# Performance work log

Hardware: AMD Instinct MI355X
Metric: run time of the kernel (lower is better)

The kernel has to match this reference:

```python
import jax, jax.numpy as jnp
import numpy as np

D_INP=36; D_MODEL=144; NHEAD=4; NHID=128; NLAYERS=2
MAX_LEN=215; D_STATIC=9; D_PE=16; N_CLASSES=2; B=128
D_OB=D_MODEL//D_INP; GCH=MAX_LEN*D_OB; D_TR=D_MODEL+D_PE; D_FINAL=D_TR+D_INP
_EI=np.stack(np.nonzero(np.ones((D_INP,D_INP),dtype=np.int64)))  # torch.nonzero(ones).T -> all pairs
SRC_N=jnp.asarray(_EI[0]); TGT_N=jnp.asarray(_EI[1]); N_EDGE=_EI.shape[1]


def setup_inputs():
    ks=jax.random.split(jax.random.key(0),40)
    def w(i,shape,s=0.05): return jax.random.normal(ks[i],shape,jnp.float32)*s
    return {
      'src': jax.random.normal(ks[0],(MAX_LEN,B,2*D_INP),jnp.float32),
      'static': jax.random.normal(ks[1],(B,D_STATIC),jnp.float32),
      'times': jax.random.uniform(ks[2],(MAX_LEN,B),jnp.float32)*MAX_LEN,
      'lengths': jax.random.randint(ks[3],(B,),32,MAX_LEN+1),
      'R_u': w(4,(1,D_INP*D_OB)),
      'emb_w': w(5,(D_INP,D_STATIC)), 'emb_b': jnp.zeros(D_INP,jnp.float32),
      'Wv1': w(6,(GCH,GCH),1.0/np.sqrt(GCH)), 'bv1': jnp.zeros(GCH,jnp.float32),
      'Wv2': w(7,(GCH,GCH),1.0/np.sqrt(GCH)), 'bv2': jnp.zeros(GCH,jnp.float32),
      'in_proj_w': w(8,(NLAYERS,3*D_TR,D_TR)), 'in_proj_b': jnp.zeros((NLAYERS,3*D_TR),jnp.float32),
      'out_w': w(9,(NLAYERS,D_TR,D_TR)), 'out_b': jnp.zeros((NLAYERS,D_TR),jnp.float32),
      'lin1_w': w(10,(NLAYERS,NHID,D_TR)), 'lin1_b': jnp.zeros((NLAYERS,NHID),jnp.float32),
      'lin2_w': w(11,(NLAYERS,D_TR,NHID)), 'lin2_b': jnp.zeros((NLAYERS,D_TR),jnp.float32),
      'ln1_s': jnp.ones((NLAYERS,D_TR),jnp.float32), 'ln1_b': jnp.zeros((NLAYERS,D_TR),jnp.float32),
      'ln2_s': jnp.ones((NLAYERS,D_TR),jnp.float32), 'ln2_b': jnp.zeros((NLAYERS,D_TR),jnp.float32),
      'mlp1_w': w(12,(D_FINAL,D_FINAL)), 'mlp1_b': jnp.zeros(D_FINAL,jnp.float32),
      'mlp2_w': w(13,(N_CLASSES,D_FINAL)), 'mlp2_b': jnp.zeros(N_CLASSES,jnp.float32),
    }


def _seg_softmax(wgt, seg, n):
    m=jnp.full((n,),-jnp.inf,wgt.dtype).at[seg].max(wgt)
    e=jnp.exp(wgt-m[seg])
    s=jnp.zeros((n,),wgt.dtype).at[seg].add(e)
    return e/s[seg]


def _ln(x,s,b):
    mu=jnp.mean(x,-1,keepdims=True); v=jnp.var(x,-1,keepdims=True)
    return (x-mu)/jnp.sqrt(v+1e-5)*s+b


def _forward(src, static, times, R_u, emb_w, emb_b, Wv1, bv1, Wv2, bv2, in_proj_w, in_proj_b, out_w, out_b, lin1_w, lin1_b, lin2_w, lin2_b, ln1_s, ln1_b, ln2_s, ln2_b, mlp1_w, mlp1_b, mlp2_w, mlp2_b, lengths):
    T,Bb=src.shape[0],src.shape[1]
    obs=src[:,:,:D_INP]                                  # drop mask half
    h=jax.nn.relu(jnp.repeat(obs,D_OB,axis=-1)*R_u)      # h_u = relu(x_u*R_u), [T,B,144]
    ts=jnp.asarray(MAX_LEN**np.linspace(0,1,D_PE//2),jnp.float32)
    scaled=times[:,:,None]/ts
    pe=jnp.concatenate([jnp.sin(scaled),jnp.cos(scaled)],-1)  # [T,B,16]
    emb=static@emb_w.T+emb_b                             # [B,36]
    # --- Observation_progation x2 (use_beta=False): gather-softmax-scatter per sensor graph ---
    xb=h.transpose(1,0,2).reshape(Bb,T,D_INP,D_OB).transpose(0,2,1,3).reshape(Bb,D_INP,GCH)
    ew=jnp.ones((N_EDGE,),jnp.float32)                   # adj=ones -> edge_weights=1
    gamma=_seg_softmax(ew,TGT_N,D_INP)                   # softmax over edges per target node
    def prop(x_,Wv,bv):
        V=jax.nn.relu(x_@Wv.T+bv)                        # relu(lin_value(x_j))
        msgs=V[:,SRC_N,:]*gamma[None,:,None]             # gather source features per edge
        return jnp.zeros_like(x_).at[:,TGT_N,:].add(msgs)  # scatter-add to targets
    x1=prop(xb,Wv1,bv1)
    x2=prop(x1,Wv2,bv2)                                  # layer2 uses alpha1 = raw edge_weights
    alpha=jnp.broadcast_to(ew[None,:],(Bb,N_EDGE))       # alpha_all.T
    sq=jnp.sum(alpha*alpha,1)
    d2=jnp.maximum(sq[:,None]+sq[None,:]-2.0*(alpha@alpha.T),0.0)
    distance=jnp.mean(jnp.sqrt(d2))
    out=x2.reshape(Bb,D_INP,T,D_OB).transpose(2,0,1,3).reshape(T,Bb,D_INP*D_OB)
    x=jnp.concatenate([out,pe],-1)                       # [T,B,160]
    mask=jnp.arange(T)[None,:]>=lengths[:,None]          # [B,T] True = padded
    hd=D_TR//NHEAD
    for l in range(NLAYERS):                             # torch post-norm TransformerEncoderLayer
        qkv=x@in_proj_w[l].T+in_proj_b[l]
        q,k,v=jnp.split(qkv,3,-1)
        def heads(t): return t.reshape(T,Bb,NHEAD,hd).transpose(1,2,0,3)  # [B,H,T,hd]
        sc=jnp.einsum('bhqd,bhkd->bhqk',heads(q),heads(k))/np.sqrt(hd)
        sc=jnp.where(mask[:,None,None,:],jnp.float32(-1e30),sc)
        o=jnp.einsum('bhqk,bhkd->bhqd',jax.nn.softmax(sc,-1),heads(v))
        o=o.transpose(2,0,1,3).reshape(T,Bb,D_TR)@out_w[l].T+out_b[l]
        x=_ln(x+o,ln1_s[l],ln1_b[l])
        ff=jax.nn.relu(x@lin1_w[l].T+lin1_b[l])@lin2_w[l].T+lin2_b[l]
        x=_ln(x+ff,ln2_s[l],ln2_b[l])
    valid=1.0-mask.T[:,:,None].astype(x.dtype)           # [T,B,1]
    agg=jnp.sum(x*valid,0)/(lengths[:,None].astype(x.dtype)+1.0)
    feat=jnp.concatenate([agg,emb],1)                    # [B,196]
    logits=jax.nn.relu(feat@mlp1_w.T+mlp1_b)@mlp2_w.T+mlp2_b
    return logits,distance


def reference(src, static, times, lengths, R_u, emb_w, emb_b, Wv1, bv1, Wv2, bv2, in_proj_w, in_proj_b, out_w, out_b, lin1_w, lin1_b, lin2_w, lin2_b, ln1_s, ln1_b, ln2_s, ln2_b, mlp1_w, mlp1_b, mlp2_w, mlp2_b):
    return _forward(src, static, times, R_u, emb_w, emb_b, Wv1, bv1, Wv2, bv2, in_proj_w, in_proj_b, out_w, out_b, lin1_w, lin1_b, lin2_w, lin2_b, ln1_s, ln1_b, ln2_s, ln2_b, mlp1_w, mlp1_b, mlp2_w, mlp2_b, lengths)
```

## Files before the change

### kernel.cpp

```cpp
#include <hip/hip_runtime.h>
#include <math.h>

#define T_LEN 215
#define TP    224
#define B_N   128
#define DINP  36
#define D_TR  160
#define HD    40
#define D_FIN 196
#define KPG   864

typedef __attribute__((ext_vector_type(8))) short short8v;
typedef __attribute__((ext_vector_type(4))) float f32x4;

__device__ __forceinline__ ushort f2bf(float x) {
  union { float f; unsigned u; } c; c.f = x;
  unsigned r = c.u + 0x7fffu + ((c.u >> 16) & 1u);
  return (ushort)(r >> 16);
}
__device__ __forceinline__ float bf2f(ushort h) {
  union { unsigned u; float f; } c; c.u = ((unsigned)h) << 16;
  return c.f;
}

__global__ __launch_bounds__(256) void k_prep(const float* __restrict__ Wv1,
    const float* __restrict__ Wv2, const float* __restrict__ ipw, const float* __restrict__ ow,
    const float* __restrict__ l1w, const float* __restrict__ l2w,
    const float* __restrict__ src, const float* __restrict__ R_u,
    const float* __restrict__ stat, const float* __restrict__ emb_w, const float* __restrict__ emb_b,
    ushort* __restrict__ wv1b, ushort* __restrict__ wv2b, ushort* __restrict__ ipwb,
    ushort* __restrict__ owb, ushort* __restrict__ l1wb, ushort* __restrict__ l2wb,
    float* __restrict__ v2acc, float* __restrict__ featacc, ushort* __restrict__ obuf16,
    ushort* __restrict__ xb16) {
  __shared__ float Ss[T_LEN * DINP];
  if (blockIdx.x >= 8202) {
    const int b = blockIdx.x - 8202, tid = threadIdx.x;
    for (int i = tid; i < T_LEN * DINP; i += 256) {
      int t = i / DINP, j = i - t * DINP;
      Ss[i] = src[((size_t)t * B_N + b) * 72 + j];
    }
    __syncthreads();
    for (int i = tid; i < DINP * T_LEN; i += 256) {
      int ii = i / T_LEN, t = i - ii * T_LEN;
      float v = Ss[t * DINP + ii];
      float4 r = ((const float4*)R_u)[ii];
      ushort4 o;
      o.x = f2bf(fmaxf(v * r.x, 0.f)); o.y = f2bf(fmaxf(v * r.y, 0.f));
      o.z = f2bf(fmaxf(v * r.z, 0.f)); o.w = f2bf(fmaxf(v * r.w, 0.f));
      ushort* row = xb16 + (size_t)(b * DINP + ii) * KPG;
      *(ushort4*)(row + 4 * t) = o;
      if (t == 0) { ushort4 z = {0, 0, 0, 0}; *(ushort4*)(row + 860) = z; }
    }
    return;
  }
  int i = blockIdx.x * 256 + threadIdx.x;
  if (i < 746496) { int n = i / KPG, k = i % KPG;
    wv1b[i] = (n < 860 && k < 860) ? f2bf(Wv1[n * 860 + k]) : (ushort)0; return; }
  i -= 746496;
  if (i < 746496) { int n = i / KPG, k = i % KPG;
    wv2b[i] = (n < 860 && k < 860) ? f2bf(Wv2[n * 860 + k]) : (ushort)0; return; }
  i -= 746496;
  if (i < 153600) { ipwb[i] = f2bf(ipw[i]); return; }
  i -= 153600;
  if (i < 51200)  { owb[i] = f2bf(ow[i]); return; }
  i -= 51200;
  if (i < 40960)  { l1wb[i] = f2bf(l1w[i]); return; }
  i -= 40960;
  if (i < 40960)  { l2wb[i] = f2bf(l2w[i]); return; }
  i -= 40960;
  if (i < 110592) { v2acc[i] = 0.f; return; }
  i -= 110592;
  if (i < 20480)  { int b = i / D_TR, d = i - b * D_TR;
    featacc[b * D_FIN + d] = 0.f; return; }
  i -= 20480;
  if (i < 4608)   { int b = i / DINP, ii = i - b * DINP;
    float s = emb_b[ii];
    #pragma unroll
    for (int k = 0; k < 9; k++) s = fmaf(stat[b * 9 + k], emb_w[ii * 9 + k], s);
    featacc[b * D_FIN + D_TR + ii] = s; return; }
  i -= 4608;
  if (i < 184320) {
    int b = i / 1440, rem = i % 1440;
    int t = 215 + rem / 160, cc = rem % 160;
    obuf16[((size_t)b * TP + t) * D_TR + cc] = 0; return;
  }
}

__global__ __launch_bounds__(256) void k_red_s1(const ushort* __restrict__ V1b, ushort* __restrict__ s1) {
  int idx = blockIdx.x * 256 + threadIdx.x;
  if (idx >= B_N * KPG) return;
  int b = idx / KPG, n = idx % KPG;
  float s = 0.f;
  if (n < 860) {
    #pragma unroll 4
    for (int i = 0; i < DINP; i++) s += bf2f(V1b[((size_t)b * DINP + i) * 860 + n]);
    s *= (1.0f / 36.0f);
  }
  s1[idx] = (n < 860) ? f2bf(s) : (ushort)0;
}

__global__ __launch_bounds__(256) void k_buildx(const float* __restrict__ v2acc,
    const float* __restrict__ bv2, const float* __restrict__ times,
    ushort* __restrict__ x16) {
  int idx = blockIdx.x * 256 + threadIdx.x;
  if (idx >= B_N * TP * 40) return;
  int c = idx % 40;
  int r = idx / 40;
  int t = r % TP, b = r / TP;
  float4 f = {0.f, 0.f, 0.f, 0.f};
  if (t < T_LEN) {
    if (c < 36) {
      float4 a = *(const float4*)&v2acc[(size_t)b * KPG + 4 * t];
      float4 bb = *(const float4*)&bv2[4 * t];
      f.x = fmaxf(a.x + bb.x, 0.f); f.y = fmaxf(a.y + bb.y, 0.f);
      f.z = fmaxf(a.z + bb.z, 0.f); f.w = fmaxf(a.w + bb.w, 0.f);
    } else {
      float tm = times[t * B_N + b];
      int j0 = (c - 36) * 4;
      bool is_sin = j0 < 8;
      int kb = j0 & 7;
      float o[4];
      #pragma unroll
      for (int qq = 0; qq < 4; qq++) {
        float ts = expf((float)(kb + qq) * 0.76723400f);
        float sc = tm / ts;
        o[qq] = is_sin ? sinf(sc) : cosf(sc);
      }
      f.x = o[0]; f.y = o[1]; f.z = o[2]; f.w = o[3];
    }
  }
  ushort4 h = {f2bf(f.x), f2bf(f.y), f2bf(f.z), f2bf(f.w)};
  *(ushort4*)(x16 + (size_t)r * D_TR + 4 * c) = h;
}

template <int RELU, int SPLIT, int WMODE, int BNT>
__global__ __launch_bounds__(256) void gemm_bf16(const ushort* __restrict__ A,
    const ushort* __restrict__ W, const float* __restrict__ bias, void* __restrict__ Cv,
    int KP, int ldc, int ncols, int kts) {
  __shared__ ushort As[128 * 32];
  __shared__ ushort Ws[BNT * 32];
  constexpr int NJ = BNT / 16;
  const int tid = threadIdx.x;
  const int wave = tid >> 6, lane = tid & 63;
  const int lr = lane & 15, hi = lane >> 4;
  const int m0 = blockIdx.y * 128, n0 = blockIdx.x * BNT;
  const int kt0 = blockIdx.z * kts;

  f32x4 acc[2][NJ];
  #pragma unroll
  for (int i = 0; i < 2; i++)
    #pragma unroll
    for (int j = 0; j < NJ; j++) acc[i][j] = (f32x4){0.f, 0.f, 0.f, 0.f};

  const int ar = tid >> 2, g = tid & 3;
  const size_t abase0 = (size_t)(m0 + ar) * KP;
  const size_t abase1 = (size_t)(m0 + ar + 64) * KP;
  const size_t bbase0 = (size_t)(n0 + ar) * KP;
  const size_t bbase1 = (size_t)(n0 + ar + 64) * KP;
  const int awb0 = ar * 64 + ((g * 16) ^ ((ar & 3) << 4));
  const int awb1 = awb0 + 64 * 64;

  const int arow0 = wave * 32 + lr;
  const int arb0 = arow0 * 64 + ((hi * 16) ^ ((arow0 & 3) << 4));
  const int arb1 = (arow0 + 16) * 64 + ((hi * 16) ^ (((arow0 + 16) & 3) << 4));
  int brb[NJ];
  #pragma unroll
  for (int j = 0; j < NJ; j++)
    brb[j] = (j * 16 + lr) * 64 + ((hi * 16) ^ ((lr & 3) << 4));

  for (int kt = 0; kt < kts; ++kt) {
    const int k0 = (kt0 + kt) * 32;
    uint4 va0 = *(const uint4*)(A + abase0 + k0 + g * 8);
    uint4 va1 = *(const uint4*)(A + abase1 + k0 + g * 8);
    uint4 vb0 = *(const uint4*)(W + bbase0 + k0 + g * 8);
    uint4 vb1;
    if constexpr (BNT == 128) vb1 = *(const uint4*)(W + bbase1 + k0 + g * 8);
    if (kt) __syncthreads();
    *(uint4*)((char*)As + awb0) = va0;
    *(uint4*)((char*)As + awb1) = va1;
    *(uint4*)((char*)Ws + awb0) = vb0;
    if constexpr (BNT == 128) *(uint4*)((char*)Ws + awb1) = vb1;
    __syncthreads();
    short8v a0 = *(const short8v*)((const char*)As + arb0);
    short8v a1 = *(const short8v*)((const char*)As + arb1);
    #pragma unroll
    for (int j = 0; j < NJ; j++) {
      short8v bf = *(const short8v*)((const char*)Ws + brb[j]);
      acc[0][j] = __builtin_amdgcn_mfma_f32_16x16x32_bf16(a0, bf, acc[0][j], 0, 0, 0);
      acc[1][j] = __builtin_amdgcn_mfma_f32_16x16x32_bf16(a1, bf, acc[1][j], 0, 0, 0);
    }
  }

  #pragma unroll
  for (int i = 0; i < 2; i++) {
    #pragma unroll
    for (int j = 0; j < NJ; j++) {
      int col = n0 + j * 16 + lr;
      int row = m0 + wave * 32 + i * 16 + hi * 4;
      if (col < ncols) {
        if (SPLIT) {
          #pragma unroll
          for (int r = 0; r < 4; r++)
            atomicAdd((float*)Cv + (size_t)(row + r) * ldc + col, acc[i][j][r]);
        } else {
          float bb = bias ? bias[col] : 0.f;
          #pragma unroll
          for (int r = 0; r < 4; r++) {
            float xv = acc[i][j][r] + bb;
            if (RELU) xv = fmaxf(xv, 0.f);
            if (WMODE == 0) ((float*)Cv)[(size_t)(row + r) * ldc + col] = xv;
            else            ((ushort*)Cv)[(size_t)(row + r) * ldc + col] = f2bf(xv);
          }
        }
      }
    }
  }
}

__global__ __launch_bounds__(256) void gemm_qkv(const ushort* __restrict__ A,
    const ushort* __restrict__ W, const float* __restrict__ bias,
    ushort* __restrict__ qkvB, ushort* __restrict__ Vt, int kts) {
  __shared__ ushort As[128 * 32];
  __shared__ ushort Ws[128 * 32];
  const int KP = 160;
  const int tid = threadIdx.x;
  const int wave = tid >> 6, lane = tid & 63;
  const int lr = lane & 15, hi = lane >> 4;
  const int m0 = blockIdx.y * 128, n0 = blockIdx.x * 128;

  f32x4 acc[2][8];
  #pragma unroll
  for (int i = 0; i < 2; i++)
    #pragma unroll
    for (int j = 0; j < 8; j++) acc[i][j] = (f32x4){0.f, 0.f, 0.f, 0.f};

  const int ar = tid >> 2, g = tid & 3;
  const size_t abase0 = (size_t)(m0 + ar) * KP;
  const size_t abase1 = (size_t)(m0 + ar + 64) * KP;
  const size_t bbase0 = (size_t)(n0 + ar) * KP;
  const size_t bbase1 = (size_t)(n0 + ar + 64) * KP;
  const int awb0 = ar * 64 + ((g * 16) ^ ((ar & 3) << 4));
  const int awb1 = awb0 + 64 * 64;

  const int arow0 = wave * 32 + lr;
  const int arb0 = arow0 * 64 + ((hi * 16) ^ ((arow0 & 3) << 4));
  const int arb1 = (arow0 + 16) * 64 + ((hi * 16) ^ (((arow0 + 16) & 3) << 4));
  int brb[8];
  #pragma unroll
  for (int j = 0; j < 8; j++)
    brb[j] = (j * 16 + lr) * 64 + ((hi * 16) ^ ((lr & 3) << 4));

  for (int kt = 0; kt < kts; ++kt) {
    const int k0 = kt * 32;
    uint4 va0 = *(const uint4*)(A + abase0 + k0 + g * 8);
    uint4 va1 = *(const uint4*)(A + abase1 + k0 + g * 8);
    uint4 vb0 = *(const uint4*)(W + bbase0 + k0 + g * 8);
    uint4 vb1 = *(const uint4*)(W + bbase1 + k0 + g * 8);
    if (kt) __syncthreads();
    *(uint4*)((char*)As + awb0) = va0;
    *(uint4*)((char*)As + awb1) = va1;
    *(uint4*)((char*)Ws + awb0) = vb0;
    *(uint4*)((char*)Ws + awb1) = vb1;
    __syncthreads();
    short8v a0 = *(const short8v*)((const char*)As + arb0);
    short8v a1 = *(const short8v*)((const char*)As + arb1);
    #pragma unroll
    for (int j = 0; j < 8; j++) {
      short8v bf = *(const short8v*)((const char*)Ws + brb[j]);
      acc[0][j] = __builtin_amdgcn_mfma_f32_16x16x32_bf16(a0, bf, acc[0][j], 0, 0, 0);
      acc[1][j] = __builtin_amdgcn_mfma_f32_16x16x32_bf16(a1, bf, acc[1][j], 0, 0, 0);
    }
  }

  #pragma unroll
  for (int i = 0; i < 2; i++) {
    const int row = m0 + wave * 32 + i * 16 + hi * 4;
    const int b = row / TP, t0 = row - b * TP;
    #pragma unroll
    for (int j = 0; j < 8; j++) {
      int col = n0 + j * 16 + lr;
      if (col < 320) {
        float bb = bias[col];
        #pragma unroll
        for (int r = 0; r < 4; r++)
          qkvB[(size_t)(row + r) * 480 + col] = f2bf(acc[i][j][r] + bb);
      } else if (col < 480) {
        float bb = bias[col];
        int dg = col - 320;
        int hh = dg / 40, dd = dg - hh * 40;
        ushort4 pv;
        pv.x = f2bf(acc[i][j][0] + bb); pv.y = f2bf(acc[i][j][1] + bb);
        pv.z = f2bf(acc[i][j][2] + bb); pv.w = f2bf(acc[i][j][3] + bb);
        *(ushort4*)(Vt + (((size_t)(b * 4 + hh) * 48 + dd) * TP + t0)) = pv;
      }
    }
  }
}

__global__ __launch_bounds__(256) void gemm_ln(const ushort* __restrict__ A,
    const ushort* __restrict__ W, const float* __restrict__ bias,
    const float* __restrict__ gam, const float* __restrict__ bet,
    ushort* __restrict__ x16, int KP, int kts,
    const int* __restrict__ lengths, float* __restrict__ featacc) {
  __shared__ ushort As[64 * 32];
  __shared__ ushort Ws[160 * 32];
  const int tid = threadIdx.x;
  const int wave = tid >> 6, lane = tid & 63;
  const int lr = lane & 15, hi = lane >> 4;
  const int m0 = blockIdx.x * 64;

  f32x4 acc[10];
  #pragma unroll
  for (int j = 0; j < 10; j++) acc[j] = (f32x4){0.f, 0.f, 0.f, 0.f};

  const int ar = tid >> 2, g = tid & 3;
  const size_t abase = (size_t)(m0 + ar) * KP;
  const int awb = ar * 64 + ((g * 16) ^ ((ar & 3) << 4));
  const int wr0 = tid >> 2,         ws0 = tid & 3;
  const int wr1 = (tid + 256) >> 2, ws1 = (tid + 256) & 3;
  const int wr2 = (tid + 512) >> 2, ws2 = (tid + 512) & 3;
  const int wwb0 = wr0 * 64 + ((ws0 * 16) ^ ((wr0 & 3) << 4));
  const int wwb1 = wr1 * 64 + ((ws1 * 16) ^ ((wr1 & 3) << 4));
  const int wwb2 = wr2 * 64 + ((ws2 * 16) ^ ((wr2 & 3) << 4));

  const int arow = wave * 16 + lr;
  const int arb = arow * 64 + ((hi * 16) ^ ((arow & 3) << 4));
  int brb[10];
  #pragma unroll
  for (int j = 0; j < 10; j++)
    brb[j] = (j * 16 + lr) * 64 + ((hi * 16) ^ ((lr & 3) << 4));

  for (int kt = 0; kt < kts; ++kt) {
    const int k0 = kt * 32;
    uint4 va = *(const uint4*)(A + abase + k0 + g * 8);
    uint4 w0 = *(const uint4*)(W + (size_t)wr0 * KP + k0 + ws0 * 8);
    uint4 w1 = *(const uint4*)(W + (size_t)wr1 * KP + k0 + ws1 * 8);
    uint4 w2;
    if (tid < 128) w2 = *(const uint4*)(W + (size_t)wr2 * KP + k0 + ws2 * 8);
    if (kt) __syncthreads();
    *(uint4*)((char*)As + awb) = va;
    *(uint4*)((char*)Ws + wwb0) = w0;
    *(uint4*)((char*)Ws + wwb1) = w1;
    if (tid < 128) *(uint4*)((char*)Ws + wwb2) = w2;
    __syncthreads();
    short8v a0 = *(const short8v*)((const char*)As + arb);
    #pragma unroll
    for (int j = 0; j < 10; j++) {
      short8v bf = *(const short8v*)((const char*)Ws + brb[j]);
      acc[j] = __builtin_amdgcn_mfma_f32_16x16x32_bf16(a0, bf, acc[j], 0, 0, 0);
    }
  }

  const int rb = m0 + wave * 16 + hi * 4;
  float s[4] = {0.f, 0.f, 0.f, 0.f};
  #pragma unroll
  for (int j = 0; j < 10; j++) {
    const int col = j * 16 + lr;
    const float bb = bias[col];
    #pragma unroll
    for (int r = 0; r < 4; r++) {
      float v = acc[j][r] + bb + bf2f(x16[(size_t)(rb + r) * D_TR + col]);
      acc[j][r] = v;
      s[r] += v;
    }
  }
  #pragma unroll
  for (int r = 0; r < 4; r++) {
    s[r] += __shfl_xor(s[r], 1, 64);
    s[r] += __shfl_xor(s[r], 2, 64);
    s[r] += __shfl_xor(s[r], 4, 64);
    s[r] += __shfl_xor(s[r], 8, 64);
  }
  float mu[4], q2[4] = {0.f, 0.f, 0.f, 0.f};
  #pragma unroll
  for (int r = 0; r < 4; r++) mu[r] = s[r] * (1.0f / 160.0f);
  #pragma unroll
  for (int j = 0; j < 10; j++)
    #pragma unroll
    for (int r = 0; r < 4; r++) {
      float d = acc[j][r] - mu[r];
      q2[r] += d * d;
    }
  #pragma unroll
  for (int r = 0; r < 4; r++) {
    q2[r] += __shfl_xor(q2[r], 1, 64);
    q2[r] += __shfl_xor(q2[r], 2, 64);
    q2[r] += __shfl_xor(q2[r], 4, 64);
    q2[r] += __shfl_xor(q2[r], 8, 64);
  }
  float rstd[4];
  #pragma unroll
  for (int r = 0; r < 4; r++) rstd[r] = rsqrtf(q2[r] * (1.0f / 160.0f) + 1e-5f);

  if (featacc == nullptr) {
    #pragma unroll
    for (int j = 0; j < 10; j++) {
      const int col = j * 16 + lr;
      const float gc = gam[col], bc = bet[col];
      #pragma unroll
      for (int r = 0; r < 4; r++) {
        float o = (acc[j][r] - mu[r]) * rstd[r] * gc + bc;
        x16[(size_t)(rb + r) * D_TR + col] = f2bf(o);
      }
    }
  } else {
    const int b = rb / TP, t0 = rb - b * TP;
    int L = lengths[b]; if (L > T_LEN) L = T_LEN;
    #pragma unroll
    for (int j = 0; j < 10; j++) {
      const int col = j * 16 + lr;
      const float gc = gam[col], bc = bet[col];
      float sacc = 0.f;
      #pragma unroll
      for (int r = 0; r < 4; r++) {
        float o = (acc[j][r] - mu[r]) * rstd[r] * gc + bc;
        if (t0 + r < L) sacc += o;
      }
      if (t0 < L) atomicAdd(&featacc[b * D_FIN + col], sacc);
    }
  }
}

__global__ __launch_bounds__(64) void k_attn4(const ushort* __restrict__ qkvB,
    const ushort* __restrict__ Vt, const int* __restrict__ lengths,
    ushort* __restrict__ o16) {
  __shared__ ushort SP[16 * 232];
  const int bh = blockIdx.x;
  const int b = bh >> 2, h = bh & 3;
  int L = lengths[b]; if (L > T_LEN) L = T_LEN;
  const int q0 = blockIdx.y << 4;
  if (q0 >= L) return;
  const int lane = threadIdx.x;
  const int lr = lane & 15, hi = lane >> 4;
  const int nk16 = (L + 15) >> 4;
  const int nkt  = (L + 31) >> 5;
  const float SC = 0.15811388300841898f;

  const ushort* qrow = qkvB + ((size_t)b * TP + q0) * 480 + h * 40;
  uint4 qa0u = *(const uint4*)(qrow + lr * 480 + hi * 8);
  uint4 qa1u = {0, 0, 0, 0};
  if (hi == 0) qa1u = *(const uint4*)(qrow + lr * 480 + 32);
  short8v qa0 = *(short8v*)&qa0u;
  short8v qa1 = *(short8v*)&qa1u;

  f32x4 c[14];
  #pragma unroll
  for (int kt = 0; kt < 14; ++kt) {
    c[kt] = (f32x4){0.f, 0.f, 0.f, 0.f};
    if (kt < nk16) {
      const ushort* krow = qkvB + ((size_t)b * TP + kt * 16) * 480 + 160 + h * 40;
      uint4 kb0u = *(const uint4*)(krow + lr * 480 + hi * 8);
      uint4 kb1u = {0, 0, 0, 0};
      if (hi == 0) kb1u = *(const uint4*)(krow + lr * 480 + 32);
      c[kt] = __builtin_amdgcn_mfma_f32_16x16x32_bf16(qa0, *(short8v*)&kb0u, c[kt], 0, 0, 0);
      c[kt] = __builtin_amdgcn_mfma_f32_16x16x32_bf16(qa1, *(short8v*)&kb1u, c[kt], 0, 0, 0);
    }
  }

  float mx[4] = {-1e30f, -1e30f, -1e30f, -1e30f};
  #pragma unroll
  for (int kt = 0; kt < 14; ++kt) {
    if (kt < nk16) {
      bool valid = (kt * 16 + lr) < L;
      #pragma unroll
      for (int r = 0; r < 4; r++) {
        float v = valid ? c[kt][r] : -1e30f;
        mx[r] = fmaxf(mx[r], v);
      }
    }
  }
  #pragma unroll
  for (int r = 0; r < 4; r++) {
    mx[r] = fmaxf(mx[r], __shfl_xor(mx[r], 1, 64));
    mx[r] = fmaxf(mx[r], __shfl_xor(mx[r], 2, 64));
    mx[r] = fmaxf(mx[r], __shfl_xor(mx[r], 4, 64));
    mx[r] = fmaxf(mx[r], __shfl_xor(mx[r], 8, 64));
  }
  float sum[4] = {0.f, 0.f, 0.f, 0.f};
  #pragma unroll
  for (int kt = 0; kt < 14; ++kt) {
    if (kt < nk16) {
      bool valid = (kt * 16 + lr) < L;
      #pragma unroll
      for (int r = 0; r < 4; r++) {
        float p = valid ? __expf(SC * (c[kt][r] - mx[r])) : 0.f;
        sum[r] += p;
        c[kt][r] = p;
      }
    }
  }
  #pragma unroll
  for (int r = 0; r < 4; r++) {
    sum[r] += __shfl_xor(sum[r], 1, 64);
    sum[r] += __shfl_xor(sum[r], 2, 64);
    sum[r] += __shfl_xor(sum[r], 4, 64);
    sum[r] += __shfl_xor(sum[r], 8, 64);
  }

  const int nk16w = nkt * 2;
  #pragma unroll
  for (int kt = 0; kt < 14; ++kt) {
    if (kt < nk16w) {
      #pragma unroll
      for (int r = 0; r < 4; r++)
        SP[(hi * 4 + r) * 232 + kt * 16 + lr] = f2bf(c[kt][r]);
    }
  }
  __syncthreads();

  f32x4 o0 = {0.f, 0.f, 0.f, 0.f}, o1 = o0, o2 = o0;
  const ushort* vbase = Vt + (size_t)bh * 48 * TP;
  #pragma unroll
  for (int kt = 0; kt < 7; ++kt) {
    if (kt < nkt) {
      short8v pa = *(const short8v*)((const char*)SP + lr * 464 + kt * 64 + hi * 16);
      const ushort* vb = vbase + kt * 32 + hi * 8;
      short8v v0 = *(const short8v*)(vb + (size_t)lr * TP);
      short8v v1 = *(const short8v*)(vb + (size_t)(16 + lr) * TP);
      short8v v2 = *(const short8v*)(vb + (size_t)(32 + lr) * TP);
      o0 = __builtin_amdgcn_mfma_f32_16x16x32_bf16(pa, v0, o0, 0, 0, 0);
      o1 = __builtin_amdgcn_mfma_f32_16x16x32_bf16(pa, v1, o1, 0, 0, 0);
      o2 = __builtin_amdgcn_mfma_f32_16x16x32_bf16(pa, v2, o2, 0, 0, 0);
    }
  }

  #pragma unroll
  for (int r = 0; r < 4; r++) {
    int t = q0 + hi * 4 + r;
    if (t < T_LEN) {
      float inv = 1.0f / sum[r];
      ushort* op = o16 + ((size_t)b * TP + t) * D_TR + h * 40;
      op[lr]      = f2bf(o0[r] * inv);
      op[16 + lr] = f2bf(o1[r] * inv);
      if (lr < 8) op[32 + lr] = f2bf(o2[r] * inv);
    }
  }
}

__global__ __launch_bounds__(256) void k_head2(const float* __restrict__ featacc,
    const int* __restrict__ lengths, const float* __restrict__ m1w,
    const float* __restrict__ m1b, const float* __restrict__ m2w,
    const float* __restrict__ m2b, float* __restrict__ out) {
  __shared__ float feat[196];
  __shared__ float m1o_s[196];
  __shared__ float r0[4], r1[4];
  const int b = blockIdx.x, tid = threadIdx.x;
  int L = lengths[b]; if (L > T_LEN) L = T_LEN;
  const float inv = 1.0f / (float)(L + 1);
  if (tid < D_FIN)
    feat[tid] = featacc[(size_t)b * D_FIN + tid] * (tid < D_TR ? inv : 1.f);
  __syncthreads();
  if (tid < D_FIN) {
    float s = m1b[tid];
    const float* wr = m1w + (size_t)tid * D_FIN;
    #pragma unroll 4
    for (int k = 0; k < D_FIN; k++) s = fmaf(feat[k], wr[k], s);
    m1o_s[tid] = fmaxf(s, 0.f);
  }
  __syncthreads();
  float p0 = 0.f, p1 = 0.f;
  if (tid < D_FIN) {
    p0 = m1o_s[tid] * m2w[tid];
    p1 = m1o_s[tid] * m2w[D_FIN + tid];
  }
  #pragma unroll
  for (int off = 32; off; off >>= 1) {
    p0 += __shfl_xor(p0, off, 64);
    p1 += __shfl_xor(p1, off, 64);
  }
  int w = tid >> 6;
  if ((tid & 63) == 0) { r0[w] = p0; r1[w] = p1; }
  __syncthreads();
  if (tid == 0) out[2 * b]     = r0[0] + r0[1] + r0[2] + r0[3] + m2b[0];
  if (tid == 1) out[2 * b + 1] = r1[0] + r1[1] + r1[2] + r1[3] + m2b[1];
  if (b == 0 && tid == 2) out[256] = 0.f;
}

extern "C" void kernel_launch(void* const* d_in, const int* in_sizes, int n_in,
                              void* d_out, int out_size, void* d_ws, size_t ws_size,
                              hipStream_t stream) {
  const float* src   = (const float*)d_in[0];
  const float* stat  = (const float*)d_in[1];
  const float* times = (const float*)d_in[2];
  const int*   lens  = (const int*)d_in[3];
  const float* R_u   = (const float*)d_in[4];
  const float* emb_w = (const float*)d_in[5];
  const float* emb_b = (const float*)d_in[6];
  const float* Wv1   = (const float*)d_in[7];
  const float* bv1   = (const float*)d_in[8];
  const float* Wv2   = (const float*)d_in[9];
  const float* bv2   = (const float*)d_in[10];
  const float* ipw   = (const float*)d_in[11];
  const float* ipb   = (const float*)d_in[12];
  const float* ow    = (const float*)d_in[13];
  const float* ob    = (const float*)d_in[14];
  const float* l1w   = (const float*)d_in[15];
  const float* l1b   = (const float*)d_in[16];
  const float* l2w   = (const float*)d_in[17];
  const float* l2b   = (const float*)d_in[18];
  const float* ln1s  = (const float*)d_in[19];
  const float* ln1bb = (const float*)d_in[20];
  const float* ln2s  = (const float*)d_in[21];
  const float* ln2bb = (const float*)d_in[22];
  const float* m1w   = (const float*)d_in[23];
  const float* m1b   = (const float*)d_in[24];
  const float* m2w   = (const float*)d_in[25];
  const float* m2b   = (const float*)d_in[26];
  float* out = (float*)d_out;

  char* p = (char*)d_ws;
  ushort* x16    = (ushort*)p;  p += 9175040;
  float*  v2acc  = (float*)p;   p += 442368;
  ushort* s1b    = (ushort*)p;  p += 221184;
  ushort* obuf16 = (ushort*)p;  p += 9175040;
  ushort* wv1b   = (ushort*)p;  p += 1492992;
  ushort* wv2b   = (ushort*)p;  p += 1492992;
  ushort* ipwb   = (ushort*)p;  p += 307200;
  ushort* owb    = (ushort*)p;  p += 102400;
  ushort* l1wb   = (ushort*)p;  p += 81920;
  ushort* l2wb   = (ushort*)p;  p += 81920;
  float*  featacc= (float*)p;   p += 100352;
  char*   R2     = p;
  ushort* xb16   = (ushort*)R2;
  ushort* V1b    = (ushort*)(R2 + 7962624);
  ushort* qkvB   = (ushort*)R2;
  ushort* ffb16  = (ushort*)R2;
  ushort* Vt     = (ushort*)(R2 + 27525120);

  k_prep<<<8330, 256, 0, stream>>>(Wv1, Wv2, ipw, ow, l1w, l2w, src, R_u,
                                   stat, emb_w, emb_b,
                                   wv1b, wv2b, ipwb, owb, l1wb, l2wb,
                                   v2acc, featacc, obuf16, xb16);

  gemm_bf16<1, 0, 1, 128><<<dim3(7, 36, 1), 256, 0, stream>>>(
      xb16, wv1b, bv1, V1b, KPG, 860, 860, 27);
  k_red_s1<<<432, 256, 0, stream>>>(V1b, s1b);
  gemm_bf16<0, 1, 0, 64><<<dim3(14, 1, 9), 256, 0, stream>>>(
      s1b, wv2b, nullptr, v2acc, KPG, KPG, KPG, 3);
  k_buildx<<<4480, 256, 0, stream>>>(v2acc, bv2, times, x16);

  for (int l = 0; l < 2; l++) {
    gemm_qkv<<<dim3(4, 224, 1), 256, 0, stream>>>(
        x16, ipwb + (size_t)l * 76800, ipb + l * 480, qkvB, Vt, 5);
    k_attn4<<<dim3(512, 14), 64, 0, stream>>>(qkvB, Vt, lens, obuf16);
    gemm_ln<<<448, 256, 0, stream>>>(obuf16, owb + (size_t)l * 25600, ob + l * 160,
                                     ln1s + l * 160, ln1bb + l * 160, x16, 160, 5,
                                     lens, nullptr);
    gemm_bf16<1, 0, 1, 64><<<dim3(2, 224, 1), 256, 0, stream>>>(
        x16, l1wb + (size_t)l * 20480, l1b + l * 128, ffb16, 160, 128, 128, 5);
    gemm_ln<<<448, 256, 0, stream>>>(ffb16, l2wb + (size_t)l * 20480, l2b + l * 160,
                                     ln2s + l * 160, ln2bb + l * 160, x16, 128, 4,
                                     lens, (l == 1) ? featacc : nullptr);
  }

  k_head2<<<128, 256, 0, stream>>>(featacc, lens, m1w, m1b, m2w, m2b, out);
}
```

Before: 248.1 us.

## Fuse node-mean reduction into GEMM epilogue and fuse FFN two-GEMM block

The first GEMM now applies bias and ReLU and atomically accumulates the mean over the 36 nodes into a float buffer, so the V1 intermediate and the separate reduction kernel are no longer needed. The second GEMM reads that float buffer directly, converting to bf16 with the 1/36 scale as it loads. In the transformer layers, lin1 and lin2 are merged into one kernel that keeps the hidden activations in shared memory, so the FFN intermediate never goes to global memory. In exchange this adds many float atomics and moves the in-place residual and LayerNorm onto the same x16 buffer that the fused FFN reads from.

After: 272.0 us. 9.6% more time.

```diff
diff --git a/kernel.cpp b/kernel.cpp
--- a/kernel.cpp
+++ b/kernel.cpp
@@ -30,11 +30,11 @@
     const float* __restrict__ stat, const float* __restrict__ emb_w, const float* __restrict__ emb_b,
     ushort* __restrict__ wv1b, ushort* __restrict__ wv2b, ushort* __restrict__ ipwb,
     ushort* __restrict__ owb, ushort* __restrict__ l1wb, ushort* __restrict__ l2wb,
-    float* __restrict__ v2acc, float* __restrict__ featacc, ushort* __restrict__ obuf16,
-    ushort* __restrict__ xb16) {
+    float* __restrict__ v2acc, float* __restrict__ s1acc, float* __restrict__ featacc,
+    ushort* __restrict__ obuf16, ushort* __restrict__ xb16) {
   __shared__ float Ss[T_LEN * DINP];
-  if (blockIdx.x >= 8202) {
-    const int b = blockIdx.x - 8202, tid = threadIdx.x;
+  if (blockIdx.x >= 8634) {
+    const int b = blockIdx.x - 8634, tid = threadIdx.x;
     for (int i = tid; i < T_LEN * DINP; i += 256) {
       int t = i / DINP, j = i - t * DINP;
       Ss[i] = src[((size_t)t * B_N + b) * 72 + j];
@@ -70,6 +70,8 @@
   i -= 40960;
   if (i < 110592) { v2acc[i] = 0.f; return; }
   i -= 110592;
+  if (i < 110592) { s1acc[i] = 0.f; return; }
+  i -= 110592;
   if (i < 20480)  { int b = i / D_TR, d = i - b * D_TR;
     featacc[b * D_FIN + d] = 0.f; return; }
   i -= 20480;
@@ -84,19 +86,6 @@
     int t = 215 + rem / 160, cc = rem % 160;
     obuf16[((size_t)b * TP + t) * D_TR + cc] = 0; return;
   }
-}
-
-__global__ __launch_bounds__(256) void k_red_s1(const ushort* __restrict__ V1b, ushort* __restrict__ s1) {
-  int idx = blockIdx.x * 256 + threadIdx.x;
-  if (idx >= B_N * KPG) return;
-  int b = idx / KPG, n = idx % KPG;
-  float s = 0.f;
-  if (n < 860) {
-    #pragma unroll 4
-    for (int i = 0; i < DINP; i++) s += bf2f(V1b[((size_t)b * DINP + i) * 860 + n]);
-    s *= (1.0f / 36.0f);
-  }
-  s1[idx] = (n < 860) ? f2bf(s) : (ushort)0;
 }
 
 __global__ __launch_bounds__(256) void k_buildx(const float* __restrict__ v2acc,
@@ -133,10 +122,10 @@
   *(ushort4*)(x16 + (size_t)r * D_TR + 4 * c) = h;
 }
 
-template <int RELU, int SPLIT, int WMODE, int BNT>
-__global__ __launch_bounds__(256) void gemm_bf16(const ushort* __restrict__ A,
+template <int RELU, int SPLIT, int WMODE, int BNT, int SOUT, int ACONV>
+__global__ __launch_bounds__(256) void gemm_bf16(const void* __restrict__ Av,
     const ushort* __restrict__ W, const float* __restrict__ bias, void* __restrict__ Cv,
-    int KP, int ldc, int ncols, int kts) {
+    int KP, int ldc, int ncols, int kts, float* __restrict__ s1acc) {
   __shared__ ushort As[128 * 32];
   __shared__ ushort Ws[BNT * 32];
   constexpr int NJ = BNT / 16;
@@ -170,8 +159,23 @@
 
   for (int kt = 0; kt < kts; ++kt) {
     const int k0 = (kt0 + kt) * 32;
-    uint4 va0 = *(const uint4*)(A + abase0 + k0 + g * 8);
-    uint4 va1 = *(const uint4*)(A + abase1 + k0 + g * 8);
+    uint4 va0, va1;
+    if constexpr (ACONV) {
+      const float* Af = (const float*)Av;
+      ushort h8[8];
+      const float* p0 = Af + abase0 + k0 + g * 8;
+      #pragma unroll
+      for (int e = 0; e < 8; e++) h8[e] = f2bf(p0[e] * (1.0f / 36.0f));
+      va0 = *(uint4*)h8;
+      const float* p1 = Af + abase1 + k0 + g * 8;
+      #pragma unroll
+      for (int e = 0; e < 8; e++) h8[e] = f2bf(p1[e] * (1.0f / 36.0f));
+      va1 = *(uint4*)h8;
+    } else {
+      const ushort* A = (const ushort*)Av;
+      va0 = *(const uint4*)(A + abase0 + k0 + g * 8);
+      va1 = *(const uint4*)(A + abase1 + k0 + g * 8);
+    }
     uint4 vb0 = *(const uint4*)(W + bbase0 + k0 + g * 8);
     uint4 vb1;
     if constexpr (BNT == 128) vb1 = *(const uint4*)(W + bbase1 + k0 + g * 8);
@@ -198,7 +202,14 @@
       int col = n0 + j * 16 + lr;
       int row = m0 + wave * 32 + i * 16 + hi * 4;
       if (col < ncols) {
-        if (SPLIT) {
+        if constexpr (SOUT) {
+          float bb = bias[col];
+          #pragma unroll
+          for (int r = 0; r < 4; r++) {
+            float xv = fmaxf(acc[i][j][r] + bb, 0.f);
+            atomicAdd(&s1acc[(size_t)((row + r) / 36) * KPG + col], xv);
+          }
+        } else if constexpr (SPLIT) {
           #pragma unroll
           for (int r = 0; r < 4; r++)
             atomicAdd((float*)Cv + (size_t)(row + r) * ldc + col, acc[i][j][r]);
@@ -357,6 +368,173 @@
   for (int j = 0; j < 10; j++) {
     const int col = j * 16 + lr;
     const float bb = bias[col];
+    #pragma unroll
+    for (int r = 0; r < 4; r++) {
+      float v = acc[j][r] + bb + bf2f(x16[(size_t)(rb + r) * D_TR + col]);
+      acc[j][r] = v;
+      s[r] += v;
+    }
+  }
+  #pragma unroll
+  for (int r = 0; r < 4; r++) {
+    s[r] += __shfl_xor(s[r], 1, 64);
+    s[r] += __shfl_xor(s[r], 2, 64);
+    s[r] += __shfl_xor(s[r], 4, 64);
+    s[r] += __shfl_xor(s[r], 8, 64);
+  }
+  float mu[4], q2[4] = {0.f, 0.f, 0.f, 0.f};
+  #pragma unroll
+  for (int r = 0; r < 4; r++) mu[r] = s[r] * (1.0f / 160.0f);
+  #pragma unroll
+  for (int j = 0; j < 10; j++)
+    #pragma unroll
+    for (int r = 0; r < 4; r++) {
+      float d = acc[j][r] - mu[r];
+      q2[r] += d * d;
+    }
+  #pragma unroll
+  for (int r = 0; r < 4; r++) {
+    q2[r] += __shfl_xor(q2[r], 1, 64);
+    q2[r] += __shfl_xor(q2[r], 2, 64);
+    q2[r] += __shfl_xor(q2[r], 4, 64);
+    q2[r] += __shfl_xor(q2[r], 8, 64);
+  }
+  float rstd[4];
+  #pragma unroll
+  for (int r = 0; r < 4; r++) rstd[r] = rsqrtf(q2[r] * (1.0f / 160.0f) + 1e-5f);
+
+  if (featacc == nullptr) {
+    #pragma unroll
+    for (int j = 0; j < 10; j++) {
+      const int col = j * 16 + lr;
+      const float gc = gam[col], bc = bet[col];
+      #pragma unroll
+      for (int r = 0; r < 4; r++) {
+        float o = (acc[j][r] - mu[r]) * rstd[r] * gc + bc;
+        x16[(size_t)(rb + r) * D_TR + col] = f2bf(o);
+      }
+    }
+  } else {
+    const int b = rb / TP, t0 = rb - b * TP;
+    int L = lengths[b]; if (L > T_LEN) L = T_LEN;
+    #pragma unroll
+    for (int j = 0; j < 10; j++) {
+      const int col = j * 16 + lr;
+      const float gc = gam[col], bc = bet[col];
+      float sacc = 0.f;
+      #pragma unroll
+      for (int r = 0; r < 4; r++) {
+        float o = (acc[j][r] - mu[r]) * rstd[r] * gc + bc;
+        if (t0 + r < L) sacc += o;
+      }
+      if (t0 < L) atomicAdd(&featacc[b * D_FIN + col], sacc);
+    }
+  }
+}
+
+__global__ __launch_bounds__(256) void gemm_ff(const ushort* __restrict__ x16in,
+    const ushort* __restrict__ W1, const float* __restrict__ b1,
+    const ushort* __restrict__ W2, const float* __restrict__ b2,
+    const float* __restrict__ gam, const float* __restrict__ bet,
+    ushort* __restrict__ x16, const int* __restrict__ lengths,
+    float* __restrict__ featacc) {
+  __shared__ ushort As[64 * 32];
+  __shared__ ushort W1s[128 * 32];
+  __shared__ ushort W2s[160 * 32];
+  __shared__ ushort Hs[64 * 136];
+  const int tid = threadIdx.x;
+  const int wave = tid >> 6, lane = tid & 63;
+  const int lr = lane & 15, hi = lane >> 4;
+  const int m0 = blockIdx.x * 64;
+
+  f32x4 acc1[8];
+  #pragma unroll
+  for (int j = 0; j < 8; j++) acc1[j] = (f32x4){0.f, 0.f, 0.f, 0.f};
+
+  const int ar = tid >> 2, g = tid & 3;
+  const size_t abase = (size_t)(m0 + ar) * 160;
+  const int awb = ar * 64 + ((g * 16) ^ ((ar & 3) << 4));
+  const int awb1 = awb + 64 * 64;
+  const size_t w1base0 = (size_t)ar * 160;
+  const size_t w1base1 = (size_t)(ar + 64) * 160;
+
+  const int arow = wave * 16 + lr;
+  const int arb = arow * 64 + ((hi * 16) ^ ((arow & 3) << 4));
+  int brb8[8];
+  #pragma unroll
+  for (int j = 0; j < 8; j++)
+    brb8[j] = (j * 16 + lr) * 64 + ((hi * 16) ^ ((lr & 3) << 4));
+
+  for (int kt = 0; kt < 5; ++kt) {
+    const int k0 = kt * 32;
+    uint4 va  = *(const uint4*)(x16in + abase + k0 + g * 8);
+    uint4 w10 = *(const uint4*)(W1 + w1base0 + k0 + g * 8);
+    uint4 w11 = *(const uint4*)(W1 + w1base1 + k0 + g * 8);
+    if (kt) __syncthreads();
+    *(uint4*)((char*)As + awb) = va;
+    *(uint4*)((char*)W1s + awb) = w10;
+    *(uint4*)((char*)W1s + awb1) = w11;
+    __syncthreads();
+    short8v a0 = *(const short8v*)((const char*)As + arb);
+    #pragma unroll
+    for (int j = 0; j < 8; j++) {
+      short8v bf = *(const short8v*)((const char*)W1s + brb8[j]);
+      acc1[j] = __builtin_amdgcn_mfma_f32_16x16x32_bf16(a0, bf, acc1[j], 0, 0, 0);
+    }
+  }
+  {
+    const int rr = wave * 16 + hi * 4;
+    #pragma unroll
+    for (int j = 0; j < 8; j++) {
+      const int col = j * 16 + lr;
+      const float bb = b1[col];
+      #pragma unroll
+      for (int r = 0; r < 4; r++)
+        Hs[(rr + r) * 136 + col] = f2bf(fmaxf(acc1[j][r] + bb, 0.f));
+    }
+  }
+  __syncthreads();
+
+  f32x4 acc[10];
+  #pragma unroll
+  for (int j = 0; j < 10; j++) acc[j] = (f32x4){0.f, 0.f, 0.f, 0.f};
+
+  const int wr0 = tid >> 2,         ws0 = tid & 3;
+  const int wr1 = (tid + 256) >> 2, ws1 = (tid + 256) & 3;
+  const int wr2 = (tid + 512) >> 2, ws2 = (tid + 512) & 3;
+  const int wwb0 = wr0 * 64 + ((ws0 * 16) ^ ((wr0 & 3) << 4));
+  const int wwb1 = wr1 * 64 + ((ws1 * 16) ^ ((wr1 & 3) << 4));
+  const int wwb2 = wr2 * 64 + ((ws2 * 16) ^ ((wr2 & 3) << 4));
+  int brb[10];
+  #pragma unroll
+  for (int j = 0; j < 10; j++)
+    brb[j] = (j * 16 + lr) * 64 + ((hi * 16) ^ ((lr & 3) << 4));
+
+  for (int kt = 0; kt < 4; ++kt) {
+    const int k0 = kt * 32;
+    uint4 w0 = *(const uint4*)(W2 + (size_t)wr0 * 128 + k0 + ws0 * 8);
+    uint4 w1 = *(const uint4*)(W2 + (size_t)wr1 * 128 + k0 + ws1 * 8);
+    uint4 w2;
+    if (tid < 128) w2 = *(const uint4*)(W2 + (size_t)wr2 * 128 + k0 + ws2 * 8);
+    if (kt) __syncthreads();
+    *(uint4*)((char*)W2s + wwb0) = w0;
+    *(uint4*)((char*)W2s + wwb1) = w1;
+    if (tid < 128) *(uint4*)((char*)W2s + wwb2) = w2;
+    __syncthreads();
+    short8v a0 = *(const short8v*)(&Hs[(wave * 16 + lr) * 136 + k0 + hi * 8]);
+    #pragma unroll
+    for (int j = 0; j < 10; j++) {
+      short8v bf = *(const short8v*)((const char*)W2s + brb[j]);
+      acc[j] = __builtin_amdgcn_mfma_f32_16x16x32_bf16(a0, bf, acc[j], 0, 0, 0);
+    }
+  }
+
+  const int rb = m0 + wave * 16 + hi * 4;
+  float s[4] = {0.f, 0.f, 0.f, 0.f};
+  #pragma unroll
+  for (int j = 0; j < 10; j++) {
+    const int col = j * 16 + lr;
+    const float bb = b2[col];
     #pragma unroll
     for (int r = 0; r < 4; r++) {
       float v = acc[j][r] + bb + bf2f(x16[(size_t)(rb + r) * D_TR + col]);
@@ -611,7 +789,7 @@
   char* p = (char*)d_ws;
   ushort* x16    = (ushort*)p;  p += 9175040;
   float*  v2acc  = (float*)p;   p += 442368;
-  ushort* s1b    = (ushort*)p;  p += 221184;
+  float*  s1acc  = (float*)p;   p += 442368;
   ushort* obuf16 = (ushort*)p;  p += 9175040;
   ushort* wv1b   = (ushort*)p;  p += 1492992;
   ushort* wv2b   = (ushort*)p;  p += 1492992;
@@ -622,21 +800,18 @@
   float*  featacc= (float*)p;   p += 100352;
   char*   R2     = p;
   ushort* xb16   = (ushort*)R2;
-  ushort* V1b    = (ushort*)(R2 + 7962624);
   ushort* qkvB   = (ushort*)R2;
-  ushort* ffb16  = (ushort*)R2;
   ushort* Vt     = (ushort*)(R2 + 27525120);
 
-  k_prep<<<8330, 256, 0, stream>>>(Wv1, Wv2, ipw, ow, l1w, l2w, src, R_u,
+  k_prep<<<8762, 256, 0, stream>>>(Wv1, Wv2, ipw, ow, l1w, l2w, src, R_u,
                                    stat, emb_w, emb_b,
                                    wv1b, wv2b, ipwb, owb, l1wb, l2wb,
-                                   v2acc, featacc, obuf16, xb16);
-
-  gemm_bf16<1, 0, 1, 128><<<dim3(7, 36, 1), 256, 0, stream>>>(
-      xb16, wv1b, bv1, V1b, KPG, 860, 860, 27);
-  k_red_s1<<<432, 256, 0, stream>>>(V1b, s1b);
-  gemm_bf16<0, 1, 0, 64><<<dim3(14, 1, 9), 256, 0, stream>>>(
-      s1b, wv2b, nullptr, v2acc, KPG, KPG, KPG, 3);
+                                   v2acc, s1acc, featacc, obuf16, xb16);
+
+  gemm_bf16<1, 0, 1, 128, 1, 0><<<dim3(7, 36, 1), 256, 0, stream>>>(
+      xb16, wv1b, bv1, nullptr, KPG, 0, 860, 27, s1acc);
+  gemm_bf16<0, 1, 0, 64, 0, 1><<<dim3(14, 1, 9), 256, 0, stream>>>(
+      s1acc, wv2b, nullptr, v2acc, KPG, KPG, KPG, 3, nullptr);
   k_buildx<<<4480, 256, 0, stream>>>(v2acc, bv2, times, x16);
 
   for (int l = 0; l < 2; l++) {
@@ -646,11 +821,10 @@
     gemm_ln<<<448, 256, 0, stream>>>(obuf16, owb + (size_t)l * 25600, ob + l * 160,
                                      ln1s + l * 160, ln1bb + l * 160, x16, 160, 5,
                                      lens, nullptr);
-    gemm_bf16<1, 0, 1, 64><<<dim3(2, 224, 1), 256, 0, stream>>>(
-        x16, l1wb + (size_t)l * 20480, l1b + l * 128, ffb16, 160, 128, 128, 5);
-    gemm_ln<<<448, 256, 0, stream>>>(ffb16, l2wb + (size_t)l * 20480, l2b + l * 160,
-                                     ln2s + l * 160, ln2bb + l * 160, x16, 128, 4,
-                                     lens, (l == 1) ? featacc : nullptr);
+    gemm_ff<<<448, 256, 0, stream>>>(x16, l1wb + (size_t)l * 20480, l1b + l * 128,
+                                     l2wb + (size_t)l * 20480, l2b + l * 160,
+                                     ln2s + l * 160, ln2bb + l * 160, x16, lens,
+                                     (l == 1) ? featacc : nullptr);
   }
 
   k_head2<<<128, 256, 0, stream>>>(featacc, lens, m1w, m1b, m2w, m2b, out);
```
